# Kernel tuning notes

Hardware: AMD Instinct MI355X
Metric: run time of the kernel (lower is better)

The kernel has to match this reference:

```python
import jax, jax.numpy as jnp
import numpy as np


def setup_inputs() -> dict:
    key = jax.random.key(0)
    ks = jax.random.split(key, 9)
    B, C, IC, H, W = 4, 128, 64, 64, 64
    s = 0.05
    return {
        "x": jax.random.normal(ks[0], (B, C, H, W), dtype=jnp.float32),
        "g_w": jax.random.normal(ks[1], (IC, C), dtype=jnp.float32) * s,
        "g_b": jax.random.normal(ks[2], (IC,), dtype=jnp.float32) * s,
        "theta_w": jax.random.normal(ks[3], (IC, C), dtype=jnp.float32) * s,
        "theta_b": jax.random.normal(ks[4], (IC,), dtype=jnp.float32) * s,
        "phi_w": jax.random.normal(ks[5], (IC, C), dtype=jnp.float32) * s,
        "phi_b": jax.random.normal(ks[6], (IC,), dtype=jnp.float32) * s,
        "W_w": jax.random.normal(ks[7], (C, IC), dtype=jnp.float32) * s,
        "W_b": jax.random.normal(ks[8], (C,), dtype=jnp.float32) * s,
    }


def reference(x, g_w, g_b, theta_w, theta_b, phi_w, phi_b, W_w, W_b):
    B, C, H, Wd = x.shape
    N = H * Wd
    xf = x.reshape(B, C, N)  # [B, C, N]
    # 1x1 convs == per-pixel channel GEMMs
    g_x = jnp.einsum('ic,bcn->bni', g_w, xf) + g_b  # [B, N, IC]
    theta_x = jnp.einsum('ic,bcn->bni', theta_w, xf) + theta_b  # [B, N, IC]
    phi_x = jnp.einsum('ic,bcn->bin', phi_w, xf) + phi_b[None, :, None]  # [B, IC, N]
    f = jnp.einsum('bni,bim->bnm', theta_x, phi_x)  # [B, N, N] (unscaled)
    f_div_C = jax.nn.softmax(f, axis=-1)
    y = jnp.einsum('bnm,bmi->bni', f_div_C, g_x)  # [B, N, IC]
    y = y.transpose(0, 2, 1)  # [B, IC, N]
    W_y = jnp.einsum('ci,bin->bcn', W_w, y) + W_b[None, :, None]  # [B, C, N]
    return (W_y + xf).reshape(B, C, H, Wd)
```

## Files before the change

kernel.cpp:

```cpp
#include <hip/hip_runtime.h>
#include <hip/hip_bf16.h>

#define BB  4
#define CC  128
#define ICH 64
#define NN  4096
#define SS  8
#define KSPLIT (NN / SS)
#define MT (KSPLIT / 64)

typedef __attribute__((ext_vector_type(4)))  float f32x4;
typedef __attribute__((ext_vector_type(16))) float f32x16;
typedef __attribute__((ext_vector_type(8)))  short bf16x8;
typedef __attribute__((ext_vector_type(4)))  unsigned u32x4;
typedef unsigned short u16;

static __device__ __forceinline__ f32x16 mfma32(bf16x8 a, bf16x8 b, f32x16 c) {
  return __builtin_amdgcn_mfma_f32_32x32x16_bf16(a, b, c, 0, 0, 0);
}
static __device__ __forceinline__ u16 f2bf(float f) {
  __hip_bfloat16 h = __float2bfloat16(f);
  return *reinterpret_cast<u16*>(&h);
}
static __device__ __forceinline__ float bf2f(u16 u) {
  union { unsigned int i; float f; } v; v.i = ((unsigned int)u) << 16; return v.f;
}
static __device__ __forceinline__ void gl_lds16(const void* g, void* l) {
  __builtin_amdgcn_global_load_lds((const __attribute__((address_space(1))) void*)g,
                                   (__attribute__((address_space(3))) void*)l, 16, 0, 0);
}
static __device__ __forceinline__ f32x16 zero16() {
  f32x16 v;
#pragma unroll
  for (int i = 0; i < 16; ++i) v[i] = 0.f;
  return v;
}
static __device__ __forceinline__ unsigned cvtpk(float lo, float hi_) {
  unsigned r;
  asm("v_cvt_pk_bf16_f32 %0, %1, %2" : "=v"(r) : "v"(lo), "v"(hi_));
  return r;
}
static __device__ __forceinline__ void pl32swap(unsigned &a, unsigned &b) {
  asm("v_permlane32_swap_b32 %0, %1" : "+v"(a), "+v"(b));
}
static __device__ __forceinline__ bf16x8 frag4(unsigned w0, unsigned w1,
                                               unsigned w2, unsigned w3) {
  union { u32x4 w; bf16x8 h; } u;
  u.w[0] = w0; u.w[1] = w1; u.w[2] = w2; u.w[3] = w3;
  return u.h;
}

__global__ __launch_bounds__(384) void proj_kernel(
    const float* __restrict__ x,
    const float* __restrict__ gw, const float* __restrict__ gb,
    const float* __restrict__ tw, const float* __restrict__ tb,
    const float* __restrict__ pw, const float* __restrict__ pb,
    u16* __restrict__ th, u16* __restrict__ ph, u16* __restrict__ gt)
{
  __shared__ __align__(16) float xs[CC * 32];
  const int t = threadIdx.x, wave = t / 64, lane = t & 63;
  const int l31 = lane & 31, hi = lane >> 5;
  const int b  = blockIdx.x >> 7;
  const int n0 = (blockIdx.x & 127) << 5;

  for (int idx = t; idx < CC * 8; idx += 384) {
    const int c = idx >> 3, n4 = idx & 7;
    *(float4*)&xs[c * 32 + n4 * 4] =
        *(const float4*)(x + ((size_t)(b * CC + c) << 12) + n0 + n4 * 4);
  }

  const int pt  = wave >> 1;
  const int ic0 = (wave & 1) << 5;
  const float* wsel = (pt == 0) ? gw : (pt == 1) ? tw : pw;

  bf16x8 wfrag[8];
  {
    const float* wrow = wsel + (ic0 + l31) * CC;
#pragma unroll
    for (int ks = 0; ks < 8; ++ks) {
      float4 a = *(const float4*)(wrow + ks * 16 + hi * 8);
      float4 c = *(const float4*)(wrow + ks * 16 + hi * 8 + 4);
      wfrag[ks] = frag4(cvtpk(a.x, a.y), cvtpk(a.z, a.w),
                        cvtpk(c.x, c.y), cvtpk(c.z, c.w));
    }
  }
  __syncthreads();

  f32x16 acc = zero16();
  if (pt == 0) {
#pragma unroll
    for (int ks = 0; ks < 8; ++ks) {
      const float* xp = xs + (ks * 16 + hi * 8) * 32 + l31;
      bf16x8 xf = frag4(cvtpk(xp[0], xp[32]),   cvtpk(xp[64], xp[96]),
                        cvtpk(xp[128], xp[160]), cvtpk(xp[192], xp[224]));
      acc = mfma32(wfrag[ks], xf, acc);
    }
#pragma unroll
    for (int reg = 0; reg < 16; ++reg) {
      const int ic = ic0 + (reg & 3) + 8 * (reg >> 2) + 4 * hi;
      gt[((size_t)(b * ICH + ic)) * NN + n0 + l31] = f2bf(acc[reg] + gb[ic]);
    }
  } else {
#pragma unroll
    for (int ks = 0; ks < 8; ++ks) {
      const float* xp = xs + (ks * 16 + hi * 8) * 32 + l31;
      bf16x8 xf = frag4(cvtpk(xp[0], xp[32]),   cvtpk(xp[64], xp[96]),
                        cvtpk(xp[128], xp[160]), cvtpk(xp[192], xp[224]));
      acc = mfma32(xf, wfrag[ks], acc);
    }
    u16* dst = (pt == 1) ? th : ph;
    const float bias = (pt == 1) ? tb[ic0 + l31] : pb[ic0 + l31];
#pragma unroll
    for (int reg = 0; reg < 16; ++reg) {
      const int n = n0 + (reg & 3) + 8 * (reg >> 2) + 4 * hi;
      dst[((size_t)(b * NN + n)) * ICH + ic0 + l31] = f2bf(acc[reg] + bias);
    }
  }
}

__global__ __launch_bounds__(256, 4) void attn_kernel(
    const u16* __restrict__ thp, const u16* __restrict__ php,
    const u16* __restrict__ gtp, u16* __restrict__ yp, float* __restrict__ Lq)
{
  __shared__ __align__(16) u16 ph_s[2][4096];
  __shared__ __align__(16) u16 gt_s[2][4096];

  const int t    = threadIdx.x;
  const int wave = t >> 6, lane = t & 63;
  const int l31  = lane & 31, hi = lane >> 5;
  const int bid  = blockIdx.x;
  const int s    = bid & 7;
  const int rb   = (bid >> 3) & 31;
  const int b    = bid >> 8;
  const int nw   = rb * 128 + wave * 32;
  const size_t bbase = (size_t)b * NN * ICH;

  const int swz  = (l31 & 7) << 4;
  const int koff = 16 * ((lane & 7) ^ (lane >> 3));

  bf16x8 aq[4];
#pragma unroll
  for (int ks = 0; ks < 4; ++ks)
    aq[ks] = *(const bf16x8*)(thp + bbase + (size_t)(nw + l31) * ICH + ks * 16 + hi * 8);

  f32x16 yacc[2];
  yacc[0] = zero16(); yacc[1] = zero16();
  float Lp = 0.f;

  const char* ph_g = (const char*)php + bbase * 2;
  const char* gt_g = (const char*)gtp + (size_t)b * ICH * NN * 2;
  const int m_start = s * KSPLIT;

  auto stage = [&](int mt, int buf) {
    const int m0 = m_start + mt * 64;
#pragma unroll
    for (int u = 0; u < 2; ++u) {
      const int kk = wave * 2 + u;
      const int row = kk * 8 + (lane >> 3);
      gl_lds16(ph_g + (size_t)(m0 + row) * 128 + koff, (char*)ph_s[buf] + kk * 1024);
      gl_lds16(gt_g + (size_t)row * (NN * 2) + m0 * 2 + koff, (char*)gt_s[buf] + kk * 1024);
    }
  };

  stage(0, 0);
  for (int mt = 0; mt < MT; ++mt) {
    __syncthreads();
    if (mt + 1 < MT) stage(mt + 1, (mt + 1) & 1);
    const char* phb = (const char*)ph_s[mt & 1];
    const char* gtb = (const char*)gt_s[mt & 1];

#pragma unroll
    for (int c = 0; c < 2; ++c) {
      bf16x8 pf4[4];
#pragma unroll
      for (int ks = 0; ks < 4; ++ks)
        pf4[ks] = *(const bf16x8*)(phb + (c * 32 + l31) * 128 +
                                   ((ks * 32 + hi * 16) ^ swz));
      f32x16 sacc = zero16();
#pragma unroll
      for (int ks = 0; ks < 4; ++ks)
        sacc = mfma32(pf4[ks], aq[ks], sacc);

      float p[16];
#pragma unroll
      for (int r = 0; r < 16; ++r) {
        p[r] = __expf(sacc[r] - 8.0f);
        Lp += p[r];
      }
      unsigned pk[8];
#pragma unroll
      for (int km = 0; km < 2; ++km) {
        unsigned P0 = cvtpk(p[km * 8 + 0], p[km * 8 + 1]);
        unsigned P1 = cvtpk(p[km * 8 + 2], p[km * 8 + 3]);
        unsigned P2 = cvtpk(p[km * 8 + 4], p[km * 8 + 5]);
        unsigned P3 = cvtpk(p[km * 8 + 6], p[km * 8 + 7]);
        pl32swap(P0, P2);
        pl32swap(P1, P3);
        pk[km * 4 + 0] = P0; pk[km * 4 + 1] = P1;
        pk[km * 4 + 2] = P2; pk[km * 4 + 3] = P3;
      }
      bf16x8 pB0 = frag4(pk[0], pk[1], pk[2], pk[3]);
      bf16x8 pB1 = frag4(pk[4], pk[5], pk[6], pk[7]);

#pragma unroll
      for (int ci = 0; ci < 2; ++ci) {
        bf16x8 gA0 = *(const bf16x8*)(gtb + (ci * 32 + l31) * 128 +
                                      ((c * 64 + 0  + hi * 16) ^ swz));
        bf16x8 gA1 = *(const bf16x8*)(gtb + (ci * 32 + l31) * 128 +
                                      ((c * 64 + 32 + hi * 16) ^ swz));
        yacc[ci] = mfma32(gA0, pB0, yacc[ci]);
        yacc[ci] = mfma32(gA1, pB1, yacc[ci]);
      }
    }
  }

  Lp += __shfl_xor(Lp, 32);

  const size_t pbase = ((size_t)s * BB + b) * NN;
  if (hi == 0) Lq[pbase + nw + l31] = Lp;

  const size_t qg = pbase + nw + l31;
#pragma unroll
  for (int ci = 0; ci < 2; ++ci)
#pragma unroll
    for (int rg = 0; rg < 4; ++rg) {
      u16 o4[4];
#pragma unroll
      for (int j = 0; j < 4; ++j) o4[j] = f2bf(yacc[ci][rg * 4 + j]);
      *(unsigned long long*)(yp + qg * ICH + ci * 32 + 8 * rg + 4 * hi) =
          *(unsigned long long*)o4;
    }
}

__global__ __launch_bounds__(256) void out_kernel(
    const float* __restrict__ x, const float* __restrict__ Ww,
    const float* __restrict__ Wb, const u16* __restrict__ yp,
    const float* __restrict__ Lq, float* __restrict__ out)
{
  __shared__ __align__(16) u16 ys[4096];
  const int t = threadIdx.x, lane = t & 63;
  const int wave = t >> 6, l31 = lane & 31, hi = lane >> 5;
  const int b  = blockIdx.x >> 7;
  const int n0 = (blockIdx.x & 127) << 5;

  {
    const int n = t >> 3, i8 = t & 7;
    float den = 0.f;
#pragma unroll
    for (int s = 0; s < SS; ++s) den += Lq[((size_t)s * BB + b) * NN + n0 + n];
    float num[8];
#pragma unroll
    for (int j = 0; j < 8; ++j) num[j] = 0.f;
#pragma unroll
    for (int s = 0; s < SS; ++s) {
      bf16x8 v = *(const bf16x8*)(yp + (((size_t)s * BB + b) * NN + n0 + n) * ICH + i8 * 8);
#pragma unroll
      for (int j = 0; j < 8; ++j) num[j] += bf2f((u16)v[j]);
    }
    float rd = 1.f / den;
    u16 o[8];
#pragma unroll
    for (int j = 0; j < 8; ++j) o[j] = f2bf(num[j] * rd);
    *(bf16x8*)((char*)ys + n * 128 + ((i8 * 16) ^ ((n & 7) << 4))) = *(bf16x8*)o;
  }
  __syncthreads();

  f32x16 acc = zero16();
  const int crow = wave * 32 + l31;
#pragma unroll
  for (int ks = 0; ks < 4; ++ks) {
    const float* wp = Ww + crow * ICH + ks * 16 + hi * 8;
    float4 w0 = *(const float4*)wp, w1 = *(const float4*)(wp + 4);
    u16 af[8];
    af[0] = f2bf(w0.x); af[1] = f2bf(w0.y); af[2] = f2bf(w0.z); af[3] = f2bf(w0.w);
    af[4] = f2bf(w1.x); af[5] = f2bf(w1.y); af[6] = f2bf(w1.z); af[7] = f2bf(w1.w);
    bf16x8 bf = *(const bf16x8*)((char*)ys + l31 * 128 +
                                 ((ks * 32 + hi * 16) ^ ((l31 & 7) << 4)));
    acc = mfma32(*(const bf16x8*)af, bf, acc);
  }
#pragma unroll
  for (int reg = 0; reg < 16; ++reg) {
    const int c = wave * 32 + (reg & 3) + 8 * (reg >> 2) + 4 * hi;
    size_t o = ((size_t)(b * CC + c) << 12) + n0 + l31;
    out[o] = acc[reg] + Wb[c] + x[o];
  }
}

extern "C" void kernel_launch(void* const* d_in, const int* in_sizes, int n_in,
                              void* d_out, int out_size, void* d_ws, size_t ws_size,
                              hipStream_t stream) {
  const float* x  = (const float*)d_in[0];
  const float* gw = (const float*)d_in[1];
  const float* gb = (const float*)d_in[2];
  const float* tw = (const float*)d_in[3];
  const float* tb = (const float*)d_in[4];
  const float* pw = (const float*)d_in[5];
  const float* pb = (const float*)d_in[6];
  const float* Ww = (const float*)d_in[7];
  const float* Wb = (const float*)d_in[8];
  float* out = (float*)d_out;

  char* ws = (char*)d_ws;
  u16*   th = (u16*)(ws);
  u16*   ph = (u16*)(ws + (2ull << 20));
  u16*   gt = (u16*)(ws + (4ull << 20));
  u16*   yp = (u16*)(ws + (6ull << 20));
  float* Lq = (float*)(ws + (22ull << 20));

  proj_kernel<<<512, 384, 0, stream>>>(x, gw, gb, tw, tb, pw, pb, th, ph, gt);
  attn_kernel<<<BB * (NN / 128) * SS, 256, 0, stream>>>(th, ph, gt, yp, Lq);
  out_kernel<<<512, 256, 0, stream>>>(x, Ww, Wb, yp, Lq, out);
}
```

Before: 57.77 us.

## Prioritize MFMA issue, hoist g loads, split out_kernel split-reduction across 512 threads

In attn_kernel, the MFMA sequences are wrapped in s_setprio so the wave gets higher issue priority. The g-tile LDS loads are hoisted ahead of the exp/pack phase so their latency overlaps the softmax math, and the row-sum is split into two accumulators to shorten the dependency chain. out_kernel doubles its block to 512 threads so each thread reduces half of the split-K partials into fp32 shared memory. The final combine and normalisation move into the MFMA operand build, which trades more LDS and a padded fp32 buffer for more memory-level parallelism in the reduction. Half of the waves sit idle during the output GEMM.

```diff
diff --git a/kernel.cpp b/kernel.cpp
--- a/kernel.cpp
+++ b/kernel.cpp
@@ -145,7 +145,7 @@
 
   f32x16 yacc[2];
   yacc[0] = zero16(); yacc[1] = zero16();
-  float Lp = 0.f;
+  float Lpa = 0.f, Lpb = 0.f;
 
   const char* ph_g = (const char*)php + bbase * 2;
   const char* gt_g = (const char*)gtp + (size_t)b * ICH * NN * 2;
@@ -177,15 +177,26 @@
         pf4[ks] = *(const bf16x8*)(phb + (c * 32 + l31) * 128 +
                                    ((ks * 32 + hi * 16) ^ swz));
       f32x16 sacc = zero16();
+      __builtin_amdgcn_s_setprio(1);
 #pragma unroll
       for (int ks = 0; ks < 4; ++ks)
         sacc = mfma32(pf4[ks], aq[ks], sacc);
+      __builtin_amdgcn_s_setprio(0);
+
+      bf16x8 gA0 = *(const bf16x8*)(gtb + (0 * 32 + l31) * 128 +
+                                    ((c * 64 + 0  + hi * 16) ^ swz));
+      bf16x8 gA1 = *(const bf16x8*)(gtb + (0 * 32 + l31) * 128 +
+                                    ((c * 64 + 32 + hi * 16) ^ swz));
+      bf16x8 gB0 = *(const bf16x8*)(gtb + (1 * 32 + l31) * 128 +
+                                    ((c * 64 + 0  + hi * 16) ^ swz));
+      bf16x8 gB1 = *(const bf16x8*)(gtb + (1 * 32 + l31) * 128 +
+                                    ((c * 64 + 32 + hi * 16) ^ swz));
 
       float p[16];
 #pragma unroll
       for (int r = 0; r < 16; ++r) {
         p[r] = __expf(sacc[r] - 8.0f);
-        Lp += p[r];
+        if (r & 1) Lpb += p[r]; else Lpa += p[r];
       }
       unsigned pk[8];
 #pragma unroll
@@ -202,18 +213,16 @@
       bf16x8 pB0 = frag4(pk[0], pk[1], pk[2], pk[3]);
       bf16x8 pB1 = frag4(pk[4], pk[5], pk[6], pk[7]);
 
-#pragma unroll
-      for (int ci = 0; ci < 2; ++ci) {
-        bf16x8 gA0 = *(const bf16x8*)(gtb + (ci * 32 + l31) * 128 +
-                                      ((c * 64 + 0  + hi * 16) ^ swz));
-        bf16x8 gA1 = *(const bf16x8*)(gtb + (ci * 32 + l31) * 128 +
-                                      ((c * 64 + 32 + hi * 16) ^ swz));
-        yacc[ci] = mfma32(gA0, pB0, yacc[ci]);
-        yacc[ci] = mfma32(gA1, pB1, yacc[ci]);
-      }
-    }
-  }
-
+      __builtin_amdgcn_s_setprio(1);
+      yacc[0] = mfma32(gA0, pB0, yacc[0]);
+      yacc[0] = mfma32(gA1, pB1, yacc[0]);
+      yacc[1] = mfma32(gB0, pB0, yacc[1]);
+      yacc[1] = mfma32(gB1, pB1, yacc[1]);
+      __builtin_amdgcn_s_setprio(0);
+    }
+  }
+
+  float Lp = Lpa + Lpb;
   Lp += __shfl_xor(Lp, 32);
 
   const size_t pbase = ((size_t)s * BB + b) * NN;
@@ -232,57 +241,70 @@
     }
 }
 
-__global__ __launch_bounds__(256) void out_kernel(
+__global__ __launch_bounds__(512) void out_kernel(
     const float* __restrict__ x, const float* __restrict__ Ww,
     const float* __restrict__ Wb, const u16* __restrict__ yp,
     const float* __restrict__ Lq, float* __restrict__ out)
 {
-  __shared__ __align__(16) u16 ys[4096];
+  __shared__ float ysf[2][32][68];
+  __shared__ float dens[2][32];
   const int t = threadIdx.x, lane = t & 63;
   const int wave = t >> 6, l31 = lane & 31, hi = lane >> 5;
   const int b  = blockIdx.x >> 7;
   const int n0 = (blockIdx.x & 127) << 5;
 
   {
-    const int n = t >> 3, i8 = t & 7;
-    float den = 0.f;
-#pragma unroll
-    for (int s = 0; s < SS; ++s) den += Lq[((size_t)s * BB + b) * NN + n0 + n];
+    const int i8 = t & 7, sh = (t >> 3) & 1, n = t >> 4;
     float num[8];
 #pragma unroll
     for (int j = 0; j < 8; ++j) num[j] = 0.f;
 #pragma unroll
-    for (int s = 0; s < SS; ++s) {
+    for (int si = 0; si < 4; ++si) {
+      const int s = sh * 4 + si;
       bf16x8 v = *(const bf16x8*)(yp + (((size_t)s * BB + b) * NN + n0 + n) * ICH + i8 * 8);
 #pragma unroll
       for (int j = 0; j < 8; ++j) num[j] += bf2f((u16)v[j]);
     }
-    float rd = 1.f / den;
-    u16 o[8];
-#pragma unroll
-    for (int j = 0; j < 8; ++j) o[j] = f2bf(num[j] * rd);
-    *(bf16x8*)((char*)ys + n * 128 + ((i8 * 16) ^ ((n & 7) << 4))) = *(bf16x8*)o;
+    *(float4*)&ysf[sh][n][i8 * 8]     = make_float4(num[0], num[1], num[2], num[3]);
+    *(float4*)&ysf[sh][n][i8 * 8 + 4] = make_float4(num[4], num[5], num[6], num[7]);
+    if (i8 == 0) {
+      float den = 0.f;
+#pragma unroll
+      for (int si = 0; si < 4; ++si)
+        den += Lq[((size_t)(sh * 4 + si) * BB + b) * NN + n0 + n];
+      dens[sh][n] = den;
+    }
   }
   __syncthreads();
 
-  f32x16 acc = zero16();
-  const int crow = wave * 32 + l31;
-#pragma unroll
-  for (int ks = 0; ks < 4; ++ks) {
-    const float* wp = Ww + crow * ICH + ks * 16 + hi * 8;
-    float4 w0 = *(const float4*)wp, w1 = *(const float4*)(wp + 4);
-    u16 af[8];
-    af[0] = f2bf(w0.x); af[1] = f2bf(w0.y); af[2] = f2bf(w0.z); af[3] = f2bf(w0.w);
-    af[4] = f2bf(w1.x); af[5] = f2bf(w1.y); af[6] = f2bf(w1.z); af[7] = f2bf(w1.w);
-    bf16x8 bf = *(const bf16x8*)((char*)ys + l31 * 128 +
-                                 ((ks * 32 + hi * 16) ^ ((l31 & 7) << 4)));
-    acc = mfma32(*(const bf16x8*)af, bf, acc);
-  }
-#pragma unroll
-  for (int reg = 0; reg < 16; ++reg) {
-    const int c = wave * 32 + (reg & 3) + 8 * (reg >> 2) + 4 * hi;
-    size_t o = ((size_t)(b * CC + c) << 12) + n0 + l31;
-    out[o] = acc[reg] + Wb[c] + x[o];
+  if (wave < 4) {
+    const float rd = 1.f / (dens[0][l31] + dens[1][l31]);
+    f32x16 acc = zero16();
+    const int crow = wave * 32 + l31;
+#pragma unroll
+    for (int ks = 0; ks < 4; ++ks) {
+      const float* wp = Ww + crow * ICH + ks * 16 + hi * 8;
+      float4 w0 = *(const float4*)wp, w1 = *(const float4*)(wp + 4);
+      u16 af[8];
+      af[0] = f2bf(w0.x); af[1] = f2bf(w0.y); af[2] = f2bf(w0.z); af[3] = f2bf(w0.w);
+      af[4] = f2bf(w1.x); af[5] = f2bf(w1.y); af[6] = f2bf(w1.z); af[7] = f2bf(w1.w);
+      const int base = ks * 16 + hi * 8;
+      float4 a0 = *(const float4*)&ysf[0][l31][base];
+      float4 a1 = *(const float4*)&ysf[0][l31][base + 4];
+      float4 b0 = *(const float4*)&ysf[1][l31][base];
+      float4 b1 = *(const float4*)&ysf[1][l31][base + 4];
+      bf16x8 bf = frag4(cvtpk((a0.x + b0.x) * rd, (a0.y + b0.y) * rd),
+                        cvtpk((a0.z + b0.z) * rd, (a0.w + b0.w) * rd),
+                        cvtpk((a1.x + b1.x) * rd, (a1.y + b1.y) * rd),
+                        cvtpk((a1.z + b1.z) * rd, (a1.w + b1.w) * rd));
+      acc = mfma32(*(const bf16x8*)af, bf, acc);
+    }
+#pragma unroll
+    for (int reg = 0; reg < 16; ++reg) {
+      const int c = wave * 32 + (reg & 3) + 8 * (reg >> 2) + 4 * hi;
+      size_t o = ((size_t)(b * CC + c) << 12) + n0 + l31;
+      out[o] = acc[reg] + Wb[c] + x[o];
+    }
   }
 }
 
@@ -309,5 +331,5 @@
 
   proj_kernel<<<512, 384, 0, stream>>>(x, gw, gb, tw, tb, pw, pb, th, ph, gt);
   attn_kernel<<<BB * (NN / 128) * SS, 256, 0, stream>>>(th, ph, gt, yp, Lq);
-  out_kernel<<<512, 256, 0, stream>>>(x, Ww, Wb, yp, Lq, out);
-}
+  out_kernel<<<512, 512, 0, stream>>>(x, Ww, Wb, yp, Lq, out);
+}
```

After: 51.76 us. 10.4% less time.
